# Kernel tuning notes

Hardware: AMD Instinct MI355X
Metric: run time of the kernel (lower is better)

Reference implementation:

```python
import jax, jax.numpy as jnp
import numpy as np
import math

B, S, D = 2, 2048, 1024
H, HKV = 16, 4
HD = D // H
NREP = H // HKV
E, TOPK, SHARED = 8, 2, 1
HIDDEN = 684
AUX_COEF = 0.01
RMS_EPS = 1e-5


def setup_inputs() -> dict:
    key = jax.random.key(0)
    ks = jax.random.split(key, 14)
    def w(k, shape):
        return jax.random.normal(k, shape, jnp.float32) * 0.02
    # standard RoPE angles, base 10000
    t = jnp.arange(S, dtype=jnp.float32)
    inv = 1.0 / (10000.0 ** (jnp.arange(0, HD, 2, dtype=jnp.float32) / HD))
    ang = t[:, None] * inv[None, :]  # [S, HD//2]
    return {
        "x": jax.random.normal(ks[0], (B, S, D), jnp.float32),
        "freqs_cos": jnp.cos(ang),
        "freqs_sin": jnp.sin(ang),
        "wq": w(ks[1], (D, D)),
        "wk": w(ks[2], (D, HKV * HD)),
        "wv": w(ks[3], (D, HKV * HD)),
        "wo": w(ks[4], (D, D)),
        "router_w": w(ks[5], (D, E)),
        "ew1": w(ks[6], (E, D, HIDDEN)),
        "ew2": w(ks[7], (E, HIDDEN, D)),
        "ew3": w(ks[8], (E, D, HIDDEN)),
        "sw1": w(ks[9], (SHARED, D, HIDDEN)),
        "sw2": w(ks[10], (SHARED, HIDDEN, D)),
        "sw3": w(ks[11], (SHARED, D, HIDDEN)),
        "g_attn": jnp.ones((D,), jnp.float32),
        "g_ffn": jnp.ones((D,), jnp.float32),
        "start_pos": 0,
    }


def rmsnorm(x, g, eps=RMS_EPS):
    xf = x.astype(jnp.float32)
    n = xf * jax.lax.rsqrt(jnp.mean(xf * xf, axis=-1, keepdims=True) + eps)
    return g * n.astype(x.dtype)


def rope(x, cos, sin):
    # pairs are consecutive elements (view_as_complex of reshape(..., -1, 2))
    xr, xi = x[..., 0::2], x[..., 1::2]
    c = cos[None, :, None, :]  # [1,S,1,HD//2]
    s = sin[None, :, None, :]
    r = xr * c - xi * s
    i = xr * s + xi * c
    return jnp.stack([r, i], axis=-1).reshape(x.shape)


def attention(x, freqs_cos, freqs_sin, wq, wk, wv, wo):
    b, s, d = x.shape
    q = (x @ wq).reshape(b, s, H, HD)
    k = (x @ wk).reshape(b, s, HKV, HD)
    v = (x @ wv).reshape(b, s, HKV, HD)
    q = rope(q, freqs_cos, freqs_sin)
    k = rope(k, freqs_cos, freqs_sin)
    k = jnp.repeat(k, NREP, axis=2)
    v = jnp.repeat(v, NREP, axis=2)
    q, k, v = (t.transpose(0, 2, 1, 3) for t in (q, k, v))  # [B,H,S,HD]
    att = jnp.einsum('bhqd,bhkd->bhqk', q, k) * (1.0 / math.sqrt(HD))
    # faithful to torch: tril then masked_fill(att == 0, -inf)
    tri = jnp.tril(jnp.ones((s, s), bool))
    att = jnp.where(tri, att, 0.0)
    att = jnp.where(att == 0.0, -jnp.inf, att)
    att = jax.nn.softmax(att, axis=-1)
    out = jnp.einsum('bhqk,bhkd->bhqd', att, v)
    out = out.transpose(0, 2, 1, 3).reshape(b, s, d)
    return out @ wo


def moe(x, router_w, ew1, ew2, ew3, sw1, sw2, sw3):
    b, s, d = x.shape
    xf = x.reshape(-1, d)                       # [N, D]
    logits = xf @ router_w                      # [N, E]
    probs = jax.nn.softmax(logits, axis=-1)
    _, topk_idx = jax.lax.top_k(logits, TOPK)   # [N, K]
    topk_p, _ = jax.lax.top_k(probs, TOPK)      # same ordering (softmax monotone)
    density = jnp.mean(jax.nn.one_hot(topk_idx[:, 0], E, dtype=jnp.float32), axis=0)
    aux = AUX_COEF * jnp.sum(density * jnp.mean(probs, axis=0)) * E
    # per-token combine weight over experts [N, E]
    onehot = jax.nn.one_hot(topk_idx, E, dtype=xf.dtype)  # [N, K, E]
    cw = jnp.einsum('nk,nke->ne', topk_p, onehot)
    # dense expert evaluation (jit-friendly dispatch/combine equivalent)
    h = jax.nn.silu(jnp.einsum('nd,edh->neh', xf, ew1)) * jnp.einsum('nd,edh->neh', xf, ew3)
    eo = jnp.einsum('neh,ehd->ned', h, ew2)
    out = jnp.einsum('ne,ned->nd', cw, eo)
    for i in range(SHARED):
        out = out + (jax.nn.silu(xf @ sw1[i]) * (xf @ sw3[i])) @ sw2[i]
    return out.reshape(b, s, d), aux


def reference(x, freqs_cos, freqs_sin, wq, wk, wv, wo, router_w, ew1, ew2, ew3, sw1, sw2, sw3, g_attn, g_ffn, start_pos):
    h = x + attention(rmsnorm(x, g_attn), freqs_cos, freqs_sin, wq, wk, wv, wo)
    ffn_out, aux = moe(rmsnorm(h, g_ffn), router_w, ew1, ew2, ew3, sw1, sw2, sw3)
    return h + ffn_out, aux
```

## Files before the change

### kernel.cpp

```cpp
#include <hip/hip_runtime.h>
#include <hip/hip_bf16.h>
#include <cstdint>

#define B_ 2
#define S_ 2048
#define D_ 1024
#define H_ 16
#define HKV_ 4
#define HD_ 64
#define E_ 8
#define HIDDEN_ 684
#define NT_ (B_*S_)
#define NEGBIG (-1e30f)

using bf16 = __hip_bfloat16;
typedef __attribute__((ext_vector_type(8))) short short8v;
typedef __attribute__((ext_vector_type(4))) short short4v;
typedef __attribute__((ext_vector_type(4))) float f32x4;

static __device__ __forceinline__ float b2f(bf16 v){ return __bfloat162float(v); }
static __device__ __forceinline__ bf16 f2b(float v){ return __float2bfloat16(v); }
static __device__ __forceinline__ short f2bs(float v){ bf16 h = f2b(v); return *reinterpret_cast<short*>(&h); }
static __device__ __forceinline__ float dload(const void* p, size_t i, int isbf){
  return isbf ? b2f(((const bf16*)p)[i]) : ((const float*)p)[i];
}

__global__ void k_detect(const uint32_t* __restrict__ g, int* __restrict__ flag, int* __restrict__ cnt){
  if(threadIdx.x == 0 && blockIdx.x == 0){
    uint32_t w0 = g[0], w1 = g[1], w2 = g[2], w3 = g[3];
    int bf;
    if(w0==0x3F803F80u && w1==0x3F803F80u && w2==0x3F803F80u && w3==0x3F803F80u) bf = 1;
    else if(w0==0x3F800000u && w1==0x3F800000u && w2==0x3F800000u && w3==0x3F800000u) bf = 0;
    else bf = 1;
    flag[0] = bf;
  }
  if(threadIdx.x < E_ && blockIdx.x == 0) cnt[threadIdx.x] = 0;
}

__global__ __launch_bounds__(256) void k_rms(const void* __restrict__ X, const void* __restrict__ g,
                                             bf16* __restrict__ outb, float* __restrict__ outf,
                                             const int* __restrict__ flag, int xdyn){
  int isbf = flag[0]; int xb = xdyn ? isbf : 0;
  int t = blockIdx.x; int tid = threadIdx.x;
  float v[4]; float ss = 0.f;
  #pragma unroll
  for(int i=0;i<4;i++){ v[i] = dload(X, (size_t)t*D_ + tid + i*256, xb); ss += v[i]*v[i]; }
  __shared__ float red[256];
  red[tid] = ss; __syncthreads();
  for(int st=128; st>0; st>>=1){ if(tid<st) red[tid] += red[tid+st]; __syncthreads(); }
  float r = rsqrtf(red[0]*(1.f/(float)D_) + 1e-5f);
  #pragma unroll
  for(int i=0;i<4;i++){
    int d = tid + i*256;
    float val = v[i]*r*dload(g, d, isbf);
    outb[(size_t)t*D_ + d] = f2b(val);
    if(outf) outf[(size_t)t*D_ + d] = val;
  }
}

#define ASTRIDE 40

static __device__ __forceinline__ f32x4 mfma16(short8v a, short8v b, f32x4 c){
  return __builtin_amdgcn_mfma_f32_16x16x32_bf16(a, b, c, 0, 0, 0);
}

template<int AMAP, int OMODE>
__global__ __launch_bounds__(256) void k_mgemm(
    const bf16* __restrict__ A, const void* __restrict__ Bw, void* __restrict__ Cout,
    const void* __restrict__ resid,
    int M, int N, int K, int ldc,
    const int* __restrict__ cnt, const int* __restrict__ offs, const int* __restrict__ list,
    const int* __restrict__ flag)
{
  int isbf = flag[0];
  int e, ct, rt;
  int base = 0; size_t eoff = 0;
  if(cnt){
    e = blockIdx.x;
    int nc = (N+63)>>6;
    ct = blockIdx.y % nc; rt = blockIdx.y / nc;
    M = cnt[e]; if(M<0) M=0; if(M>NT_) M=NT_;
    base = offs[e];
    eoff = (size_t)e*(size_t)K*(size_t)N;
  } else {
    e = 0; ct = blockIdx.x; rt = blockIdx.y;
  }
  int m0 = rt*128; if(m0 >= M) return;
  int n0 = ct*64;

  __shared__ short As[2][128*ASTRIDE];
  __shared__ short Bs[2][64*ASTRIDE];
  __shared__ int rowA[128];

  int tid = threadIdx.x;
  int w = tid>>6, l = tid&63, lr = l&15, lg = l>>4;

  if(tid < 128){
    int rloc = m0 + tid;
    int ar = -1;
    if(rloc < M) ar = (AMAP==2) ? (list[e*NT_ + rloc]>>1) : (base + rloc);
    rowA[tid] = ar;
  }
  __syncthreads();

  int srow = tid>>1, skh = (tid&1)*16;
  int keya = (srow>>4)&3, kb0 = skh>>3;
  int bk = tid>>3, bnc = (tid&7)*8;
  int keyb = ((tid&7)>>1)&3;
  int bcol = (((bk>>3)^keyb)<<3) + (bk&7);
  int arow = rowA[srow];

  short8v rA0, rA1, rB;

  auto loadAB = [&](int kt){
    int k0 = kt*32;
    {
      short tmp[16];
      if(arow >= 0 && k0+skh+16 <= K){
        const short4v* src = (const short4v*)(A + (size_t)arow*K + k0 + skh);
        #pragma unroll
        for(int c=0;c<4;c++) *(short4v*)&tmp[c*4] = src[c];
      } else {
        #pragma unroll
        for(int i=0;i<16;i++){
          int gk = k0+skh+i;
          short v = 0;
          if(arow>=0 && gk<K) v = *(const short*)&A[(size_t)arow*K+gk];
          tmp[i] = v;
        }
      }
      #pragma unroll
      for(int i=0;i<8;i++){ rA0[i]=tmp[i]; rA1[i]=tmp[8+i]; }
    }
    {
      int gk = k0 + bk;
      short tmp[8];
      if(gk < K && n0+bnc+8 <= N){
        size_t bb = eoff + (size_t)gk*N + n0 + bnc;
        if(isbf){
          const short4v* src = (const short4v*)((const bf16*)Bw + bb);
          *(short4v*)&tmp[0] = src[0];
          *(short4v*)&tmp[4] = src[1];
        } else {
          const f32x4* src = (const f32x4*)((const float*)Bw + bb);
          f32x4 f0 = src[0], f1 = src[1];
          #pragma unroll
          for(int i=0;i<4;i++){ tmp[i]=f2bs(f0[i]); tmp[4+i]=f2bs(f1[i]); }
        }
      } else {
        #pragma unroll
        for(int i=0;i<8;i++){
          int gn = n0+bnc+i;
          float v = 0.f;
          if(gk<K && gn<N) v = dload(Bw, eoff + (size_t)gk*N + gn, isbf);
          tmp[i] = f2bs(v);
        }
      }
      #pragma unroll
      for(int i=0;i<8;i++) rB[i]=tmp[i];
    }
  };
  auto writeAB = [&](int buf){
    *(short8v*)&As[buf][srow*ASTRIDE + ((kb0^keya)<<3)]     = rA0;
    *(short8v*)&As[buf][srow*ASTRIDE + (((kb0+1)^keya)<<3)] = rA1;
    #pragma unroll
    for(int i=0;i<8;i++) Bs[buf][(bnc+i)*ASTRIDE + bcol] = rB[i];
  };

  f32x4 acc[2][4] = {};
  int KT = (K+31)>>5;

  loadAB(0); writeAB(0);
  __syncthreads();
  int cur = 0;
  for(int kt=0; kt<KT; ++kt){
    bool more = (kt+1 < KT);
    if(more) loadAB(kt+1);
    short8v a[2], b[4];
    #pragma unroll
    for(int fi=0;fi<2;fi++)
      a[fi] = *(const short8v*)&As[cur][(w*32+fi*16+lr)*ASTRIDE + ((lg^((w*2+fi)&3))<<3)];
    #pragma unroll
    for(int fj=0;fj<4;fj++)
      b[fj] = *(const short8v*)&Bs[cur][(fj*16+lr)*ASTRIDE + ((lg^fj)<<3)];
    #pragma unroll
    for(int fi=0;fi<2;fi++)
      #pragma unroll
      for(int fj=0;fj<4;fj++)
        acc[fi][fj] = mfma16(a[fi], b[fj], acc[fi][fj]);
    if(more){ writeAB(cur^1); cur ^= 1; }
    __syncthreads();
  }

  #pragma unroll
  for(int fi=0;fi<2;fi++){
    #pragma unroll
    for(int r=0;r<4;r++){
      int rl = m0 + w*32 + fi*16 + lg*4 + r;
      if(rl >= M) continue;
      int orow;
      if(OMODE==2){ orow = list[e*NT_ + rl]; if(orow<0||orow>=2*NT_) continue; }
      else orow = base + rl;
      #pragma unroll
      for(int fj=0;fj<4;fj++){
        int gcol = n0 + fj*16 + lr;
        if(gcol >= N) continue;
        float v = acc[fi][fj][r];
        size_t o = (size_t)orow*ldc + gcol;
        if(OMODE==1)      ((float*)Cout)[o] = v + dload(resid, o, isbf);
        else if(OMODE==2) ((bf16*)Cout)[o] = f2b(v);
        else if(OMODE==3) ((float*)Cout)[o] = ((float*)Cout)[o] + v;
        else              ((bf16*)Cout)[o] = f2b(v);
      }
    }
  }
}

__global__ __launch_bounds__(256) void k_qkv(
    const bf16* __restrict__ A, const void* __restrict__ Wq, const void* __restrict__ Wk,
    const void* __restrict__ Wv, bf16* __restrict__ Oq, bf16* __restrict__ Ok, bf16* __restrict__ Ov,
    const void* __restrict__ fc, const void* __restrict__ fs,
    const int* __restrict__ flag)
{
  int isbf = flag[0];
  int ct = blockIdx.x, rt = blockIdx.y;
  const void* Bw; bf16* Cout; int N, n0;
  if(ct < 16){ Bw = Wq; Cout = Oq; N = D_;  n0 = ct*64; }
  else if(ct < 20){ Bw = Wk; Cout = Ok; N = 256; n0 = (ct-16)*64; }
  else { Bw = Wv; Cout = Ov; N = 256; n0 = (ct-20)*64; }
  const int K = D_, M = NT_;
  int m0 = rt*128;
  int dorope = (ct < 20);

  __shared__ short As[2][128*ASTRIDE];
  __shared__ short Bs[2][64*ASTRIDE];

  int tid = threadIdx.x;
  int w = tid>>6, l = tid&63, lr = l&15, lg = l>>4;

  int srow = tid>>1, skh = (tid&1)*16;
  int keya = (srow>>4)&3, kb0 = skh>>3;
  int bk = tid>>3, bnc = (tid&7)*8;
  int keyb = ((tid&7)>>1)&3;
  int bcol = (((bk>>3)^keyb)<<3) + (bk&7);
  int arow = m0 + srow;

  short8v rA0, rA1, rB;

  auto loadAB = [&](int kt){
    int k0 = kt*32;
    {
      short tmp[16];
      const short4v* src = (const short4v*)(A + (size_t)arow*K + k0 + skh);
      #pragma unroll
      for(int c=0;c<4;c++) *(short4v*)&tmp[c*4] = src[c];
      #pragma unroll
      for(int i=0;i<8;i++){ rA0[i]=tmp[i]; rA1[i]=tmp[8+i]; }
    }
    {
      int gk = k0 + bk;
      short tmp[8];
      size_t bb = (size_t)gk*N + n0 + bnc;
      if(isbf){
        const short4v* src = (const short4v*)((const bf16*)Bw + bb);
        *(short4v*)&tmp[0] = src[0];
        *(short4v*)&tmp[4] = src[1];
      } else {
        const f32x4* src = (const f32x4*)((const float*)Bw + bb);
        f32x4 f0 = src[0], f1 = src[1];
        #pragma unroll
        for(int i=0;i<4;i++){ tmp[i]=f2bs(f0[i]); tmp[4+i]=f2bs(f1[i]); }
      }
      #pragma unroll
      for(int i=0;i<8;i++) rB[i]=tmp[i];
    }
  };
  auto writeAB = [&](int buf){
    *(short8v*)&As[buf][srow*ASTRIDE + ((kb0^keya)<<3)]     = rA0;
    *(short8v*)&As[buf][srow*ASTRIDE + (((kb0+1)^keya)<<3)] = rA1;
    #pragma unroll
    for(int i=0;i<8;i++) Bs[buf][(bnc+i)*ASTRIDE + bcol] = rB[i];
  };

  f32x4 acc[2][4] = {};
  int KT = K>>5;

  loadAB(0); writeAB(0);
  __syncthreads();
  int cur = 0;
  for(int kt=0; kt<KT; ++kt){
    bool more = (kt+1 < KT);
    if(more) loadAB(kt+1);
    short8v a[2], b[4];
    #pragma unroll
    for(int fi=0;fi<2;fi++)
      a[fi] = *(const short8v*)&As[cur][(w*32+fi*16+lr)*ASTRIDE + ((lg^((w*2+fi)&3))<<3)];
    #pragma unroll
    for(int fj=0;fj<4;fj++)
      b[fj] = *(const short8v*)&Bs[cur][(fj*16+lr)*ASTRIDE + ((lg^fj)<<3)];
    #pragma unroll
    for(int fi=0;fi<2;fi++)
      #pragma unroll
      for(int fj=0;fj<4;fj++)
        acc[fi][fj] = mfma16(a[fi], b[fj], acc[fi][fj]);
    if(more){ writeAB(cur^1); cur ^= 1; }
    __syncthreads();
  }

  #pragma unroll
  for(int fi=0;fi<2;fi++){
    #pragma unroll
    for(int r=0;r<4;r++){
      int rl = m0 + w*32 + fi*16 + lg*4 + r;
      int s = rl & (S_-1);
      #pragma unroll
      for(int fj=0;fj<4;fj++){
        int gcol = n0 + fj*16 + lr;
        float v = acc[fi][fj][r];
        if(dorope){
          float partner = __shfl_xor(v, 1, 64);
          int p = (gcol & 63) >> 1;
          float c = dload(fc, s*32 + p, isbf);
          float sn = dload(fs, s*32 + p, isbf);
          if((l & 1) == 0) v = v*c - partner*sn;
          else             v = partner*sn + v*c;
        }
        Cout[(size_t)rl*N + gcol] = f2b(v);
      }
    }
  }
}

__global__ __launch_bounds__(256) void k_ffn1m(
    const bf16* __restrict__ A, const void* __restrict__ W1e, const void* __restrict__ W3e,
    const void* __restrict__ W1s, const void* __restrict__ W3s,
    bf16* __restrict__ OutE, bf16* __restrict__ OutS,
    const int* __restrict__ cnt, const int* __restrict__ offs, const int* __restrict__ list,
    const int* __restrict__ flag)
{
  int isbf = flag[0];
  const int K = D_, N = HIDDEN_;
  int e = blockIdx.x, y = blockIdx.y;
  int ct, rt, M, base, gat;
  const void* W1; const void* W3; bf16* Out;
  size_t eoff;
  if(y < 352){
    ct = y % 11; rt = y / 11;
    M = cnt[e]; if(M<0) M=0; if(M>NT_) M=NT_;
    base = offs[e]; gat = 1;
    W1 = W1e; W3 = W3e; Out = OutE;
    eoff = (size_t)e*(size_t)K*(size_t)N;
  } else {
    int ys = (y-352)*8 + e;
    ct = ys % 11; rt = ys / 11;
    M = NT_; base = 0; gat = 0;
    W1 = W1s; W3 = W3s; Out = OutS;
    eoff = 0;
  }
  int m0 = rt*128; if(m0 >= M) return;
  int n0 = ct*64;

  __shared__ short As[2][128*ASTRIDE];
  __shared__ short B1s[2][64*ASTRIDE];
  __shared__ short B3s[2][64*ASTRIDE];
  __shared__ int rowA[128];

  int tid = threadIdx.x;
  int w = tid>>6, l = tid&63, lr = l&15, lg = l>>4;

  if(tid < 128){
    int rloc = m0 + tid;
    int ar = -1;
    if(rloc < M) ar = gat ? (list[e*NT_ + rloc]>>1) : rloc;
    rowA[tid] = ar;
  }
  __syncthreads();

  int srow = tid>>1, skh = (tid&1)*16;
  int keya = (srow>>4)&3, kb0 = skh>>3;
  int bk = tid>>3, bnc = (tid&7)*8;
  int keyb = ((tid&7)>>1)&3;
  int bcol = (((bk>>3)^keyb)<<3) + (bk&7);
  int arow = rowA[srow];

  short8v rA0, rA1, rB1, rB3;

  auto loadB = [&](const void* Bw, int kt, short8v& rB){
    int k0 = kt*32;
    int gk = k0 + bk;
    short tmp[8];
    if(gk < K && n0+bnc+8 <= N){
      size_t bb = eoff + (size_t)gk*N + n0 + bnc;
      if(isbf){
        const short4v* src = (const short4v*)((const bf16*)Bw + bb);
        *(short4v*)&tmp[0] = src[0];
        *(short4v*)&tmp[4] = src[1];
      } else {
        const f32x4* src = (const f32x4*)((const float*)Bw + bb);
        f32x4 f0 = src[0], f1 = src[1];
        #pragma unroll
        for(int i=0;i<4;i++){ tmp[i]=f2bs(f0[i]); tmp[4+i]=f2bs(f1[i]); }
      }
    } else {
      #pragma unroll
      for(int i=0;i<8;i++){
        int gn = n0+bnc+i;
        float v = 0.f;
        if(gk<K && gn<N) v = dload(Bw, eoff + (size_t)gk*N + gn, isbf);
        tmp[i] = f2bs(v);
      }
    }
    #pragma unroll
    for(int i=0;i<8;i++) rB[i]=tmp[i];
  };
  auto loadA = [&](int kt){
    int k0 = kt*32;
    short tmp[16];
    if(arow >= 0 && k0+skh+16 <= K){
      const short4v* src = (const short4v*)(A + (size_t)arow*K + k0 + skh);
      #pragma unroll
      for(int c=0;c<4;c++) *(short4v*)&tmp[c*4] = src[c];
    } else {
      #pragma unroll
      for(int i=0;i<16;i++){
        int gk = k0+skh+i;
        short v = 0;
        if(arow>=0 && gk<K) v = *(const short*)&A[(size_t)arow*K+gk];
        tmp[i] = v;
      }
    }
    #pragma unroll
    for(int i=0;i<8;i++){ rA0[i]=tmp[i]; rA1[i]=tmp[8+i]; }
  };
  auto writeAll = [&](int buf){
    *(short8v*)&As[buf][srow*ASTRIDE + ((kb0^keya)<<3)]     = rA0;
    *(short8v*)&As[buf][srow*ASTRIDE + (((kb0+1)^keya)<<3)] = rA1;
    #pragma unroll
    for(int i=0;i<8;i++){
      B1s[buf][(bnc+i)*ASTRIDE + bcol] = rB1[i];
      B3s[buf][(bnc+i)*ASTRIDE + bcol] = rB3[i];
    }
  };

  f32x4 a1[2][4] = {}, a3[2][4] = {};
  int KT = (K+31)>>5;

  loadA(0); loadB(W1, 0, rB1); loadB(W3, 0, rB3); writeAll(0);
  __syncthreads();
  int cur = 0;
  for(int kt=0; kt<KT; ++kt){
    bool more = (kt+1 < KT);
    if(more){ loadA(kt+1); loadB(W1, kt+1, rB1); loadB(W3, kt+1, rB3); }
    short8v a[2], b1[4], b3[4];
    #pragma unroll
    for(int fi=0;fi<2;fi++)
      a[fi] = *(const short8v*)&As[cur][(w*32+fi*16+lr)*ASTRIDE + ((lg^((w*2+fi)&3))<<3)];
    #pragma unroll
    for(int fj=0;fj<4;fj++){
      b1[fj] = *(const short8v*)&B1s[cur][(fj*16+lr)*ASTRIDE + ((lg^fj)<<3)];
      b3[fj] = *(const short8v*)&B3s[cur][(fj*16+lr)*ASTRIDE + ((lg^fj)<<3)];
    }
    #pragma unroll
    for(int fi=0;fi<2;fi++)
      #pragma unroll
      for(int fj=0;fj<4;fj++){
        a1[fi][fj] = mfma16(a[fi], b1[fj], a1[fi][fj]);
        a3[fi][fj] = mfma16(a[fi], b3[fj], a3[fi][fj]);
      }
    if(more){ writeAll(cur^1); cur ^= 1; }
    __syncthreads();
  }

  #pragma unroll
  for(int fi=0;fi<2;fi++){
    #pragma unroll
    for(int r=0;r<4;r++){
      int rl = m0 + w*32 + fi*16 + lg*4 + r;
      if(rl >= M) continue;
      int orow = base + rl;
      #pragma unroll
      for(int fj=0;fj<4;fj++){
        int gcol = n0 + fj*16 + lr;
        if(gcol >= N) continue;
        float sg = a1[fi][fj][r];
        float v = (sg/(1.f+__expf(-sg))) * a3[fi][fj][r];
        Out[(size_t)orow*N + gcol] = f2b(v);
      }
    }
  }
}

__global__ __launch_bounds__(256) void k_ffn2m(
    const bf16* __restrict__ Ae, const bf16* __restrict__ Ash,
    const void* __restrict__ W2e, const void* __restrict__ W2s,
    bf16* __restrict__ OutE, float* __restrict__ OutS,
    const int* __restrict__ cnt, const int* __restrict__ offs, const int* __restrict__ list,
    const int* __restrict__ flag)
{
  int isbf = flag[0];
  const int K = HIDDEN_, N = D_;
  int e = blockIdx.x, y = blockIdx.y;
  int ct, rt, M, base, exm;
  const bf16* A; const void* Bw;
  size_t eoff;
  if(y < 256){
    ct = y % 8; rt = y / 8;
    M = cnt[e]; if(M<0) M=0; if(M>NT_) M=NT_;
    base = offs[e]; exm = 1;
    A = Ae; Bw = W2e;
    eoff = (size_t)e*(size_t)K*(size_t)N;
  } else {
    int ys = (y-256)*8 + e;
    ct = ys % 8; rt = ys / 8;
    M = NT_; base = 0; exm = 0;
    A = Ash; Bw = W2s;
    eoff = 0;
  }
  int m0 = rt*128; if(m0 >= M) return;
  int n0 = ct*128;

  __shared__ short As[128*ASTRIDE];
  __shared__ short Bs[128*ASTRIDE];

  int tid = threadIdx.x;
  int w = tid>>6, l = tid&63, lr = l&15, lg = l>>4;

  int srow = tid>>1, skh = (tid&1)*16;
  int keya = (srow>>4)&3, kb0 = skh>>3;
  int bk = tid>>3, bnc = (tid&7)*16;
  int keyb = (tid&7)&3;
  int bcol = (((bk>>3)^keyb)<<3) + (bk&7);
  int arow = (m0 + srow < M) ? (base + m0 + srow) : -1;

  short8v rA0, rA1, rB0v, rB1v;

  auto loadAB = [&](int kt){
    int k0 = kt*32;
    {
      short tmp[16];
      if(arow >= 0 && k0+skh+16 <= K){
        const short4v* src = (const short4v*)(A + (size_t)arow*K + k0 + skh);
        #pragma unroll
        for(int c=0;c<4;c++) *(short4v*)&tmp[c*4] = src[c];
      } else {
        #pragma unroll
        for(int i=0;i<16;i++){
          int gk = k0+skh+i;
          short v = 0;
          if(arow>=0 && gk<K) v = *(const short*)&A[(size_t)arow*K+gk];
          tmp[i] = v;
        }
      }
      #pragma unroll
      for(int i=0;i<8;i++){ rA0[i]=tmp[i]; rA1[i]=tmp[8+i]; }
    }
    {
      int gk = k0 + bk;
      short tmp[16];
      if(gk < K){
        size_t bb = eoff + (size_t)gk*N + n0 + bnc;
        if(isbf){
          const short4v* src = (const short4v*)((const bf16*)Bw + bb);
          #pragma unroll
          for(int c=0;c<4;c++) *(short4v*)&tmp[c*4] = src[c];
        } else {
          const f32x4* src = (const f32x4*)((const float*)Bw + bb);
          #pragma unroll
          for(int c=0;c<4;c++){
            f32x4 f = src[c];
            #pragma unroll
            for(int i=0;i<4;i++) tmp[c*4+i] = f2bs(f[i]);
          }
        }
      } else {
        #pragma unroll
        for(int i=0;i<16;i++) tmp[i] = 0;
      }
      #pragma unroll
      for(int i=0;i<8;i++){ rB0v[i]=tmp[i]; rB1v[i]=tmp[8+i]; }
    }
  };
  auto writeAB = [&](){
    *(short8v*)&As[srow*ASTRIDE + ((kb0^keya)<<3)]     = rA0;
    *(short8v*)&As[srow*ASTRIDE + (((kb0+1)^keya)<<3)] = rA1;
    #pragma unroll
    for(int i=0;i<8;i++) Bs[(bnc+i)*ASTRIDE + bcol]   = rB0v[i];
    #pragma unroll
    for(int i=0;i<8;i++) Bs[(bnc+8+i)*ASTRIDE + bcol] = rB1v[i];
  };

  f32x4 acc[2][8] = {};
  int KT = (K+31)>>5;

  loadAB(0); writeAB();
  __syncthreads();
  for(int kt=0; kt<KT; ++kt){
    bool more = (kt+1 < KT);
    if(more) loadAB(kt+1);
    short8v a[2], b[8];
    #pragma unroll
    for(int fi=0;fi<2;fi++)
      a[fi] = *(const short8v*)&As[(w*32+fi*16+lr)*ASTRIDE + ((lg^((w*2+fi)&3))<<3)];
    #pragma unroll
    for(int fj=0;fj<8;fj++)
      b[fj] = *(const short8v*)&Bs[(fj*16+lr)*ASTRIDE + ((lg^(fj&3))<<3)];
    #pragma unroll
    for(int fi=0;fi<2;fi++)
      #pragma unroll
      for(int fj=0;fj<8;fj++)
        acc[fi][fj] = mfma16(a[fi], b[fj], acc[fi][fj]);
    __syncthreads();
    if(more){ writeAB(); __syncthreads(); }
  }

  #pragma unroll
  for(int fi=0;fi<2;fi++){
    #pragma unroll
    for(int r=0;r<4;r++){
      int rl = m0 + w*32 + fi*16 + lg*4 + r;
      if(rl >= M) continue;
      if(exm){
        int orow = list[e*NT_ + rl];
        if(orow<0||orow>=2*NT_) continue;
        #pragma unroll
        for(int fj=0;fj<8;fj++){
          int gcol = n0 + fj*16 + lr;
          OutE[(size_t)orow*N + gcol] = f2b(acc[fi][fj][r]);
        }
      } else {
        #pragma unroll
        for(int fj=0;fj<8;fj++){
          int gcol = n0 + fj*16 + lr;
          size_t o = (size_t)rl*N + gcol;
          OutS[o] = OutS[o] + acc[fi][fj][r];
        }
      }
    }
  }
}

#define TST 72

__global__ __launch_bounds__(256) void k_attn(const bf16* __restrict__ Q, const bf16* __restrict__ Kg,
                                              const bf16* __restrict__ V, bf16* __restrict__ Out){
  int qt_ = (S_/64 - 1) - blockIdx.x;
  int h = blockIdx.y, b = blockIdx.z;
  int kvh = h>>2;
  const bf16* qb = Q + (size_t)b*S_*D_ + h*HD_;
  const bf16* kb = Kg + (size_t)b*S_*256 + kvh*HD_;
  const bf16* vb = V  + (size_t)b*S_*256 + kvh*HD_;
  __shared__ short Qs[64*TST];
  __shared__ short Ks[64*TST];
  __shared__ short Vt[64*TST];
  __shared__ short Ps[4][16*TST];
  int tid = threadIdx.x;
  int w = tid>>6, l = tid&63, lr = l&15, lg = l>>4;
  int sr = tid>>2, sc0 = (tid&3)*16;
  int vc = (((sr>>3)^(tid&3))<<3) + (sr&7);

  {
    const short8v* src = (const short8v*)(qb + (size_t)(qt_*64 + sr)*D_ + sc0);
    *(short8v*)&Qs[sr*TST + sc0]     = src[0];
    *(short8v*)&Qs[sr*TST + sc0 + 8] = src[1];
  }
  __syncthreads();
  short8v aQ0 = *(const short8v*)&Qs[(w*16+lr)*TST + lg*8];
  short8v aQ1 = *(const short8v*)&Qs[(w*16+lr)*TST + lg*8 + 32];

  float mreg[4], lreg[4];
  f32x4 accO[4] = {};
  #pragma unroll
  for(int r=0;r<4;r++){ mreg[r] = NEGBIG; lreg[r] = 0.f; }

  for(int kt=0; kt<=qt_; ++kt){
    __syncthreads();
    {
      const short8v* ksrc = (const short8v*)(kb + (size_t)(kt*64 + sr)*256 + sc0);
      *(short8v*)&Ks[sr*TST + sc0]     = ksrc[0];
      *(short8v*)&Ks[sr*TST + sc0 + 8] = ksrc[1];
      const short8v* vsrc = (const short8v*)(vb + (size_t)(kt*64 + sr)*256 + sc0);
      short8v v0 = vsrc[0], v1 = vsrc[1];
      #pragma unroll
      for(int i=0;i<8;i++){
        Vt[(sc0+i)*TST + vc]   = v0[i];
        Vt[(sc0+8+i)*TST + vc] = v1[i];
      }
    }
    __syncthreads();
    f32x4 s[4];
    #pragma unroll
    for(int fj=0; fj<4; fj++){
      short8v b0 = *(const short8v*)&Ks[(fj*16+lr)*TST + lg*8];
      short8v b1 = *(const short8v*)&Ks[(fj*16+lr)*TST + lg*8 + 32];
      f32x4 z = {};
      z = mfma16(aQ0, b0, z);
      z = mfma16(aQ1, b1, z);
      s[fj] = z;
    }
    #pragma unroll
    for(int fj=0; fj<4; fj++)
      #pragma unroll
      for(int r=0;r<4;r++){
        float v = s[fj][r]*0.125f;
        if(kt==qt_ && (fj*16+lr) > (w*16+lg*4+r)) v = NEGBIG;
        s[fj][r] = v;
      }
    float p[4][4], sc[4];
    #pragma unroll
    for(int r=0;r<4;r++){
      float mx = fmaxf(fmaxf(s[0][r],s[1][r]), fmaxf(s[2][r],s[3][r]));
      mx = fmaxf(mx, __shfl_xor(mx,1,64));
      mx = fmaxf(mx, __shfl_xor(mx,2,64));
      mx = fmaxf(mx, __shfl_xor(mx,4,64));
      mx = fmaxf(mx, __shfl_xor(mx,8,64));
      float mn = fmaxf(mreg[r], mx);
      sc[r] = __expf(mreg[r]-mn);
      float ps = 0.f;
      #pragma unroll
      for(int fj=0;fj<4;fj++){ float pv = __expf(s[fj][r]-mn); p[fj][r] = pv; ps += pv; }
      ps += __shfl_xor(ps,1,64); ps += __shfl_xor(ps,2,64);
      ps += __shfl_xor(ps,4,64); ps += __shfl_xor(ps,8,64);
      lreg[r] = lreg[r]*sc[r] + ps;
      mreg[r] = mn;
    }
    #pragma unroll
    for(int fj=0;fj<4;fj++)
      #pragma unroll
      for(int r=0;r<4;r++)
        accO[fj][r] *= sc[r];
    #pragma unroll
    for(int fj=0;fj<4;fj++)
      #pragma unroll
      for(int r=0;r<4;r++)
        Ps[w][(lg*4+r)*TST + fj*16+lr] = f2bs(p[fj][r]);
    short8v a0 = *(const short8v*)&Ps[w][lr*TST + lg*8];
    short8v a1 = *(const short8v*)&Ps[w][lr*TST + lg*8 + 32];
    #pragma unroll
    for(int fj=0;fj<4;fj++){
      int row = fj*16+lr;
      short8v b0 = *(const short8v*)&Vt[row*TST + ((lg^fj)<<3)];
      short8v b1 = *(const short8v*)&Vt[row*TST + (((lg^fj)+4)<<3)];
      accO[fj] = mfma16(a0, b0, accO[fj]);
      accO[fj] = mfma16(a1, b1, accO[fj]);
    }
  }
  #pragma unroll
  for(int r=0;r<4;r++){
    int qr = qt_*64 + w*16 + lg*4 + r;
    float inv = (lreg[r] > 0.f) ? 1.f/lreg[r] : 0.f;
    #pragma unroll
    for(int fj=0;fj<4;fj++)
      Out[((size_t)(b*S_+qr))*D_ + h*HD_ + fj*16+lr] = f2b(accO[fj][r]*inv);
  }
}

__global__ __launch_bounds__(64) void k_router(const float* __restrict__ X, const void* __restrict__ W,
                                               float* __restrict__ probs, float* __restrict__ p01,
                                               int* __restrict__ idx0buf, int* __restrict__ list,
                                               int* __restrict__ cnt, const int* __restrict__ flag){
  int isbf = flag[0];
  int t = blockIdx.x; int lane = threadIdx.x;
  float pe[8] = {};
  if(isbf){
    const bf16* Wb = (const bf16*)W;
    for(int d = lane; d < D_; d += 64){
      float xv = X[(size_t)t*D_ + d];
      #pragma unroll
      for(int e=0;e<8;e++) pe[e] += xv*b2f(Wb[(size_t)d*E_+e]);
    }
  } else {
    const float* Wf = (const float*)W;
    for(int d = lane; d < D_; d += 64){
      float xv = X[(size_t)t*D_ + d];
      #pragma unroll
      for(int e=0;e<8;e++) pe[e] += xv*Wf[(size_t)d*E_+e];
    }
  }
  for(int msk=1;msk<64;msk<<=1)
    #pragma unroll
    for(int e=0;e<8;e++) pe[e] += __shfl_xor(pe[e], msk, 64);
  if(lane == 0){
    float mx = pe[0];
    #pragma unroll
    for(int e=1;e<8;e++) mx = fmaxf(mx, pe[e]);
    float pr[8], sum = 0.f;
    #pragma unroll
    for(int e=0;e<8;e++){ pr[e] = __expf(pe[e]-mx); sum += pr[e]; }
    #pragma unroll
    for(int e=0;e<8;e++){ pr[e] /= sum; probs[t*8+e] = pr[e]; }
    int i0 = 0;
    #pragma unroll
    for(int e=1;e<8;e++) if(pe[e] > pe[i0]) i0 = e;
    int i1 = -1;
    #pragma unroll
    for(int e=0;e<8;e++){ if(e==i0) continue; if(i1<0 || pe[e] > pe[i1]) i1 = e; }
    p01[t*2]   = pr[i0];
    p01[t*2+1] = pr[i1];
    idx0buf[t] = i0;
    int pos = atomicAdd(&cnt[i0], 1);
    if(pos >= 0 && pos < NT_) list[i0*NT_ + pos] = t*2;
    pos     = atomicAdd(&cnt[i1], 1);
    if(pos >= 0 && pos < NT_) list[i1*NT_ + pos] = t*2 + 1;
  }
}

__global__ __launch_bounds__(256) void k_stats(const float* __restrict__ probs, const int* __restrict__ idx0buf,
                                               float* __restrict__ cnt0f, float* __restrict__ psum){
  int e = blockIdx.x; int tid = threadIdx.x;
  float sp = 0.f, sc = 0.f;
  for(int n = tid; n < NT_; n += 256){ sp += probs[n*8+e]; sc += (idx0buf[n]==e) ? 1.f : 0.f; }
  __shared__ float r1[256], r2[256];
  r1[tid] = sp; r2[tid] = sc; __syncthreads();
  for(int st=128; st>0; st>>=1){ if(tid<st){ r1[tid]+=r1[tid+st]; r2[tid]+=r2[tid+st]; } __syncthreads(); }
  if(tid==0){ psum[e] = r1[0]; cnt0f[e] = r2[0]; }
}

__global__ void k_finish(const float* __restrict__ cnt0f, const float* __restrict__ psum,
                         const int* __restrict__ cnt, int* __restrict__ offs,
                         bf16* __restrict__ auxb, float* __restrict__ auxf, const int* __restrict__ flag){
  if(threadIdx.x==0 && blockIdx.x==0){
    int o = 0;
    for(int e=0;e<8;e++){ offs[e] = o; int c = cnt[e]; if(c < 0) c = 0; if(c > NT_) c = NT_; o += c; }
    float aux = 0.f;
    for(int e=0;e<8;e++) aux += (cnt0f[e]*(1.f/(float)NT_))*(psum[e]*(1.f/(float)NT_));
    float v = aux*0.01f*8.f;
    if(flag[0]) auxb[0] = f2b(v); else auxf[0] = v;
  }
}

__global__ __launch_bounds__(256) void k_combine(const float* __restrict__ hbuf, const bf16* __restrict__ eosl,
                                                 const float* __restrict__ p01,
                                                 bf16* __restrict__ outb, float* __restrict__ outf,
                                                 const int* __restrict__ flag){
  int t = blockIdx.x; int tid = threadIdx.x;
  int isbf = flag[0];
  float p0 = p01[t*2], p1 = p01[t*2+1];
  #pragma unroll
  for(int i=0;i<4;i++){
    int d = tid + i*256;
    float v = hbuf[(size_t)t*D_ + d]
            + p0*b2f(eosl[((size_t)(t*2))*D_ + d])
            + p1*b2f(eosl[((size_t)(t*2+1))*D_ + d]);
    size_t o = (size_t)t*D_ + d;
    if(isbf) outb[o] = f2b(v); else outf[o] = v;
  }
}

static const size_t O_HBUF = 0;
static const size_t O_XNB  = 16777216;
static const size_t O_QLIN = 25165824;
static const size_t O_KLIN = 33554432;
static const size_t O_VLIN = 35651584;
static const size_t O_AOUT = 37748736;
static const size_t O_XN2B = 16777216;
static const size_t O_XN2F = 25165824;
static const size_t O_HEXP = 46137344;
static const size_t O_SHH  = 57344000;
static const size_t O_EOSL = 16777216;
static const size_t O_PROBS= 62947328;
static const size_t O_P01  = 63078400;
static const size_t O_IDX0 = 63111168;
static const size_t O_LIST = 63127552;
static const size_t O_CNT  = 63258624;
static const size_t O_CNT0 = 63258656;
static const size_t O_PSUM = 63258688;
static const size_t O_OFFS = 63258720;
static const size_t O_FLAG = 63258752;

extern "C" void kernel_launch(void* const* d_in, const int* in_sizes, int n_in,
                              void* d_out, int out_size, void* d_ws, size_t ws_size,
                              hipStream_t stream){
  (void)in_sizes; (void)n_in; (void)out_size; (void)ws_size;
  char* ws = (char*)d_ws;
  float* hbuf = (float*)(ws + O_HBUF);
  bf16* xnb   = (bf16*)(ws + O_XNB);
  bf16* qlin  = (bf16*)(ws + O_QLIN);
  bf16* klin  = (bf16*)(ws + O_KLIN);
  bf16* vlin  = (bf16*)(ws + O_VLIN);
  bf16* aout  = (bf16*)(ws + O_AOUT);
  bf16* xn2b  = (bf16*)(ws + O_XN2B);
  float* xn2f = (float*)(ws + O_XN2F);
  bf16* hexp  = (bf16*)(ws + O_HEXP);
  bf16* shh   = (bf16*)(ws + O_SHH);
  bf16* eosl  = (bf16*)(ws + O_EOSL);
  float* probs=(float*)(ws + O_PROBS);
  float* p01 = (float*)(ws + O_P01);
  int*  idx0 = (int*)(ws + O_IDX0);
  int*  list = (int*)(ws + O_LIST);
  int*  cnt  = (int*)(ws + O_CNT);
  float* cnt0f=(float*)(ws + O_CNT0);
  float* psum= (float*)(ws + O_PSUM);
  int*  offs = (int*)(ws + O_OFFS);
  int*  flg  = (int*)(ws + O_FLAG);

  bf16* outb = (bf16*)d_out;
  float* outf = (float*)d_out;
  bf16* auxb = outb + (size_t)NT_*D_;
  float* auxf = outf + (size_t)NT_*D_;

  k_detect<<<1, 64, 0, stream>>>((const uint32_t*)d_in[14], flg, cnt);

  k_rms<<<NT_, 256, 0, stream>>>(d_in[0], d_in[14], xnb, nullptr, flg, 1);

  k_qkv<<<dim3(24,32), 256, 0, stream>>>(xnb, d_in[3], d_in[4], d_in[5], qlin, klin, vlin,
                                         d_in[1], d_in[2], flg);

  k_attn<<<dim3(S_/64, H_, B_), 256, 0, stream>>>(qlin, klin, vlin, aout);

  k_mgemm<0,1><<<dim3(16,32), 256, 0, stream>>>(aout, d_in[6], hbuf, d_in[0], NT_, D_, D_, D_, nullptr, nullptr, nullptr, flg);

  k_rms<<<NT_, 256, 0, stream>>>(hbuf, d_in[15], xn2b, xn2f, flg, 0);

  k_router<<<NT_, 64, 0, stream>>>(xn2f, d_in[7], probs, p01, idx0, list, cnt, flg);
  k_stats<<<E_, 256, 0, stream>>>(probs, idx0, cnt0f, psum);
  k_finish<<<1, 64, 0, stream>>>(cnt0f, psum, cnt, offs, auxb, auxf, flg);

  k_ffn1m<<<dim3(E_, 352+44), 256, 0, stream>>>(xn2b, d_in[8], d_in[10], d_in[11], d_in[13],
                                                hexp, shh, cnt, offs, list, flg);

  k_ffn2m<<<dim3(E_, 256+32), 256, 0, stream>>>(hexp, shh, d_in[9], d_in[12],
                                                eosl, hbuf, cnt, offs, list, flg);

  k_combine<<<NT_, 256, 0, stream>>>(hbuf, eosl, p01, outb, outf, flg);
}
```

Measured before the change: 617.2 us.

## Widen QKV and Wo GEMM tiles to 128x128 with single-buffered LDS

The QKV projection and the output-projection GEMMs now use 128x128 output tiles instead of 128x64, so each wave holds twice as many accumulators and each A tile is reused across more columns. Shared memory drops from double to single buffering, with an extra barrier before writing the next tile. The generic templated k_mgemm is replaced by a specialized k_wo kernel with no bounds checks. The trade-off is fewer blocks (384 and 256) on a large GPU, higher register pressure, and less overlap between loads and MFMA.

```diff
diff --git a/kernel.cpp b/kernel.cpp
--- a/kernel.cpp
+++ b/kernel.cpp
@@ -64,132 +64,93 @@
   return __builtin_amdgcn_mfma_f32_16x16x32_bf16(a, b, c, 0, 0, 0);
 }
 
-template<int AMAP, int OMODE>
-__global__ __launch_bounds__(256) void k_mgemm(
-    const bf16* __restrict__ A, const void* __restrict__ Bw, void* __restrict__ Cout,
-    const void* __restrict__ resid,
-    int M, int N, int K, int ldc,
-    const int* __restrict__ cnt, const int* __restrict__ offs, const int* __restrict__ list,
-    const int* __restrict__ flag)
+__global__ __launch_bounds__(256) void k_wo(
+    const bf16* __restrict__ A, const void* __restrict__ Bw, float* __restrict__ Cout,
+    const void* __restrict__ resid, const int* __restrict__ flag)
 {
   int isbf = flag[0];
-  int e, ct, rt;
-  int base = 0; size_t eoff = 0;
-  if(cnt){
-    e = blockIdx.x;
-    int nc = (N+63)>>6;
-    ct = blockIdx.y % nc; rt = blockIdx.y / nc;
-    M = cnt[e]; if(M<0) M=0; if(M>NT_) M=NT_;
-    base = offs[e];
-    eoff = (size_t)e*(size_t)K*(size_t)N;
-  } else {
-    e = 0; ct = blockIdx.x; rt = blockIdx.y;
-  }
-  int m0 = rt*128; if(m0 >= M) return;
-  int n0 = ct*64;
-
-  __shared__ short As[2][128*ASTRIDE];
-  __shared__ short Bs[2][64*ASTRIDE];
-  __shared__ int rowA[128];
+  const int K = D_, N = D_, M = NT_;
+  int ct = blockIdx.x, rt = blockIdx.y;
+  int m0 = rt*128;
+  int n0 = ct*128;
+
+  __shared__ short As[128*ASTRIDE];
+  __shared__ short Bs[128*ASTRIDE];
 
   int tid = threadIdx.x;
   int w = tid>>6, l = tid&63, lr = l&15, lg = l>>4;
 
-  if(tid < 128){
-    int rloc = m0 + tid;
-    int ar = -1;
-    if(rloc < M) ar = (AMAP==2) ? (list[e*NT_ + rloc]>>1) : (base + rloc);
-    rowA[tid] = ar;
-  }
-  __syncthreads();
-
   int srow = tid>>1, skh = (tid&1)*16;
   int keya = (srow>>4)&3, kb0 = skh>>3;
-  int bk = tid>>3, bnc = (tid&7)*8;
-  int keyb = ((tid&7)>>1)&3;
+  int bk = tid>>3, bnc = (tid&7)*16;
+  int keyb = (tid&7)&3;
   int bcol = (((bk>>3)^keyb)<<3) + (bk&7);
-  int arow = rowA[srow];
-
-  short8v rA0, rA1, rB;
+  int arow = m0 + srow;
+
+  short8v rA0, rA1, rB0v, rB1v;
 
   auto loadAB = [&](int kt){
     int k0 = kt*32;
     {
       short tmp[16];
-      if(arow >= 0 && k0+skh+16 <= K){
-        const short4v* src = (const short4v*)(A + (size_t)arow*K + k0 + skh);
+      const short4v* src = (const short4v*)(A + (size_t)arow*K + k0 + skh);
+      #pragma unroll
+      for(int c=0;c<4;c++) *(short4v*)&tmp[c*4] = src[c];
+      #pragma unroll
+      for(int i=0;i<8;i++){ rA0[i]=tmp[i]; rA1[i]=tmp[8+i]; }
+    }
+    {
+      int gk = k0 + bk;
+      short tmp[16];
+      size_t bb = (size_t)gk*N + n0 + bnc;
+      if(isbf){
+        const short4v* src = (const short4v*)((const bf16*)Bw + bb);
         #pragma unroll
         for(int c=0;c<4;c++) *(short4v*)&tmp[c*4] = src[c];
       } else {
-        #pragma unroll
-        for(int i=0;i<16;i++){
-          int gk = k0+skh+i;
-          short v = 0;
-          if(arow>=0 && gk<K) v = *(const short*)&A[(size_t)arow*K+gk];
-          tmp[i] = v;
+        const f32x4* src = (const f32x4*)((const float*)Bw + bb);
+        #pragma unroll
+        for(int c=0;c<4;c++){
+          f32x4 f = src[c];
+          #pragma unroll
+          for(int i=0;i<4;i++) tmp[c*4+i] = f2bs(f[i]);
         }
       }
       #pragma unroll
-      for(int i=0;i<8;i++){ rA0[i]=tmp[i]; rA1[i]=tmp[8+i]; }
-    }
-    {
-      int gk = k0 + bk;
-      short tmp[8];
-      if(gk < K && n0+bnc+8 <= N){
-        size_t bb = eoff + (size_t)gk*N + n0 + bnc;
-        if(isbf){
-          const short4v* src = (const short4v*)((const bf16*)Bw + bb);
-          *(short4v*)&tmp[0] = src[0];
-          *(short4v*)&tmp[4] = src[1];
-        } else {
-          const f32x4* src = (const f32x4*)((const float*)Bw + bb);
-          f32x4 f0 = src[0], f1 = src[1];
-          #pragma unroll
-          for(int i=0;i<4;i++){ tmp[i]=f2bs(f0[i]); tmp[4+i]=f2bs(f1[i]); }
-        }
-      } else {
-        #pragma unroll
-        for(int i=0;i<8;i++){
-          int gn = n0+bnc+i;
-          float v = 0.f;
-          if(gk<K && gn<N) v = dload(Bw, eoff + (size_t)gk*N + gn, isbf);
-          tmp[i] = f2bs(v);
-        }
-      }
-      #pragma unroll
-      for(int i=0;i<8;i++) rB[i]=tmp[i];
+      for(int i=0;i<8;i++){ rB0v[i]=tmp[i]; rB1v[i]=tmp[8+i]; }
     }
   };
-  auto writeAB = [&](int buf){
-    *(short8v*)&As[buf][srow*ASTRIDE + ((kb0^keya)<<3)]     = rA0;
-    *(short8v*)&As[buf][srow*ASTRIDE + (((kb0+1)^keya)<<3)] = rA1;
-    #pragma unroll
-    for(int i=0;i<8;i++) Bs[buf][(bnc+i)*ASTRIDE + bcol] = rB[i];
+  auto writeAB = [&](){
+    *(short8v*)&As[srow*ASTRIDE + ((kb0^keya)<<3)]     = rA0;
+    *(short8v*)&As[srow*ASTRIDE + (((kb0+1)^keya)<<3)] = rA1;
+    #pragma unroll
+    for(int i=0;i<8;i++) Bs[(bnc+i)*ASTRIDE + bcol]   = rB0v[i];
+    #pragma unroll
+    for(int i=0;i<8;i++) Bs[(bnc+8+i)*ASTRIDE + bcol] = rB1v[i];
   };
 
-  f32x4 acc[2][4] = {};
-  int KT = (K+31)>>5;
-
-  loadAB(0); writeAB(0);
+  f32x4 acc[2][8] = {};
+  int KT = K>>5;
+
+  loadAB(0); writeAB();
   __syncthreads();
-  int cur = 0;
   for(int kt=0; kt<KT; ++kt){
     bool more = (kt+1 < KT);
     if(more) loadAB(kt+1);
-    short8v a[2], b[4];
+    short8v a[2], b[8];
     #pragma unroll
     for(int fi=0;fi<2;fi++)
-      a[fi] = *(const short8v*)&As[cur][(w*32+fi*16+lr)*ASTRIDE + ((lg^((w*2+fi)&3))<<3)];
-    #pragma unroll
-    for(int fj=0;fj<4;fj++)
-      b[fj] = *(const short8v*)&Bs[cur][(fj*16+lr)*ASTRIDE + ((lg^fj)<<3)];
+      a[fi] = *(const short8v*)&As[(w*32+fi*16+lr)*ASTRIDE + ((lg^((w*2+fi)&3))<<3)];
+    #pragma unroll
+    for(int fj=0;fj<8;fj++)
+      b[fj] = *(const short8v*)&Bs[(fj*16+lr)*ASTRIDE + ((lg^(fj&3))<<3)];
     #pragma unroll
     for(int fi=0;fi<2;fi++)
       #pragma unroll
-      for(int fj=0;fj<4;fj++)
+      for(int fj=0;fj<8;fj++)
         acc[fi][fj] = mfma16(a[fi], b[fj], acc[fi][fj]);
-    if(more){ writeAB(cur^1); cur ^= 1; }
     __syncthreads();
+    if(more){ writeAB(); __syncthreads(); }
   }
 
   #pragma unroll
@@ -197,20 +158,11 @@
     #pragma unroll
     for(int r=0;r<4;r++){
       int rl = m0 + w*32 + fi*16 + lg*4 + r;
-      if(rl >= M) continue;
-      int orow;
-      if(OMODE==2){ orow = list[e*NT_ + rl]; if(orow<0||orow>=2*NT_) continue; }
-      else orow = base + rl;
-      #pragma unroll
-      for(int fj=0;fj<4;fj++){
+      #pragma unroll
+      for(int fj=0;fj<8;fj++){
         int gcol = n0 + fj*16 + lr;
-        if(gcol >= N) continue;
-        float v = acc[fi][fj][r];
-        size_t o = (size_t)orow*ldc + gcol;
-        if(OMODE==1)      ((float*)Cout)[o] = v + dload(resid, o, isbf);
-        else if(OMODE==2) ((bf16*)Cout)[o] = f2b(v);
-        else if(OMODE==3) ((float*)Cout)[o] = ((float*)Cout)[o] + v;
-        else              ((bf16*)Cout)[o] = f2b(v);
+        size_t o = (size_t)rl*N + gcol;
+        Cout[o] = acc[fi][fj][r] + dload(resid, o, isbf);
       }
     }
   }
@@ -225,27 +177,27 @@
   int isbf = flag[0];
   int ct = blockIdx.x, rt = blockIdx.y;
   const void* Bw; bf16* Cout; int N, n0;
-  if(ct < 16){ Bw = Wq; Cout = Oq; N = D_;  n0 = ct*64; }
-  else if(ct < 20){ Bw = Wk; Cout = Ok; N = 256; n0 = (ct-16)*64; }
-  else { Bw = Wv; Cout = Ov; N = 256; n0 = (ct-20)*64; }
+  if(ct < 8){ Bw = Wq; Cout = Oq; N = D_;  n0 = ct*128; }
+  else if(ct < 10){ Bw = Wk; Cout = Ok; N = 256; n0 = (ct-8)*128; }
+  else { Bw = Wv; Cout = Ov; N = 256; n0 = (ct-10)*128; }
   const int K = D_, M = NT_;
   int m0 = rt*128;
-  int dorope = (ct < 20);
-
-  __shared__ short As[2][128*ASTRIDE];
-  __shared__ short Bs[2][64*ASTRIDE];
+  int dorope = (ct < 10);
+
+  __shared__ short As[128*ASTRIDE];
+  __shared__ short Bs[128*ASTRIDE];
 
   int tid = threadIdx.x;
   int w = tid>>6, l = tid&63, lr = l&15, lg = l>>4;
 
   int srow = tid>>1, skh = (tid&1)*16;
   int keya = (srow>>4)&3, kb0 = skh>>3;
-  int bk = tid>>3, bnc = (tid&7)*8;
-  int keyb = ((tid&7)>>1)&3;
+  int bk = tid>>3, bnc = (tid&7)*16;
+  int keyb = (tid&7)&3;
   int bcol = (((bk>>3)^keyb)<<3) + (bk&7);
   int arow = m0 + srow;
 
-  short8v rA0, rA1, rB;
+  short8v rA0, rA1, rB0v, rB1v;
 
   auto loadAB = [&](int kt){
     int k0 = kt*32;
@@ -259,52 +211,56 @@
     }
     {
       int gk = k0 + bk;
-      short tmp[8];
+      short tmp[16];
       size_t bb = (size_t)gk*N + n0 + bnc;
       if(isbf){
         const short4v* src = (const short4v*)((const bf16*)Bw + bb);
-        *(short4v*)&tmp[0] = src[0];
-        *(short4v*)&tmp[4] = src[1];
+        #pragma unroll
+        for(int c=0;c<4;c++) *(short4v*)&tmp[c*4] = src[c];
       } else {
         const f32x4* src = (const f32x4*)((const float*)Bw + bb);
-        f32x4 f0 = src[0], f1 = src[1];
-        #pragma unroll
-        for(int i=0;i<4;i++){ tmp[i]=f2bs(f0[i]); tmp[4+i]=f2bs(f1[i]); }
-      }
-      #pragma unroll
-      for(int i=0;i<8;i++) rB[i]=tmp[i];
+        #pragma unroll
+        for(int c=0;c<4;c++){
+          f32x4 f = src[c];
+          #pragma unroll
+          for(int i=0;i<4;i++) tmp[c*4+i] = f2bs(f[i]);
+        }
+      }
+      #pragma unroll
+      for(int i=0;i<8;i++){ rB0v[i]=tmp[i]; rB1v[i]=tmp[8+i]; }
     }
   };
-  auto writeAB = [&](int buf){
-    *(short8v*)&As[buf][srow*ASTRIDE + ((kb0^keya)<<3)]     = rA0;
-    *(short8v*)&As[buf][srow*ASTRIDE + (((kb0+1)^keya)<<3)] = rA1;
-    #pragma unroll
-    for(int i=0;i<8;i++) Bs[buf][(bnc+i)*ASTRIDE + bcol] = rB[i];
+  auto writeAB = [&](){
+    *(short8v*)&As[srow*ASTRIDE + ((kb0^keya)<<3)]     = rA0;
+    *(short8v*)&As[srow*ASTRIDE + (((kb0+1)^keya)<<3)] = rA1;
+    #pragma unroll
+    for(int i=0;i<8;i++) Bs[(bnc+i)*ASTRIDE + bcol]   = rB0v[i];
+    #pragma unroll
+    for(int i=0;i<8;i++) Bs[(bnc+8+i)*ASTRIDE + bcol] = rB1v[i];
   };
 
-  f32x4 acc[2][4] = {};
+  f32x4 acc[2][8] = {};
   int KT = K>>5;
 
-  loadAB(0); writeAB(0);
+  loadAB(0); writeAB();
   __syncthreads();
-  int cur = 0;
   for(int kt=0; kt<KT; ++kt){
     bool more = (kt+1 < KT);
     if(more) loadAB(kt+1);
-    short8v a[2], b[4];
+    short8v a[2], b[8];
     #pragma unroll
     for(int fi=0;fi<2;fi++)
-      a[fi] = *(const short8v*)&As[cur][(w*32+fi*16+lr)*ASTRIDE + ((lg^((w*2+fi)&3))<<3)];
-    #pragma unroll
-    for(int fj=0;fj<4;fj++)
-      b[fj] = *(const short8v*)&Bs[cur][(fj*16+lr)*ASTRIDE + ((lg^fj)<<3)];
+      a[fi] = *(const short8v*)&As[(w*32+fi*16+lr)*ASTRIDE + ((lg^((w*2+fi)&3))<<3)];
+    #pragma unroll
+    for(int fj=0;fj<8;fj++)
+      b[fj] = *(const short8v*)&Bs[(fj*16+lr)*ASTRIDE + ((lg^(fj&3))<<3)];
     #pragma unroll
     for(int fi=0;fi<2;fi++)
       #pragma unroll
-      for(int fj=0;fj<4;fj++)
+      for(int fj=0;fj<8;fj++)
         acc[fi][fj] = mfma16(a[fi], b[fj], acc[fi][fj]);
-    if(more){ writeAB(cur^1); cur ^= 1; }
     __syncthreads();
+    if(more){ writeAB(); __syncthreads(); }
   }
 
   #pragma unroll
@@ -314,7 +270,7 @@
       int rl = m0 + w*32 + fi*16 + lg*4 + r;
       int s = rl & (S_-1);
       #pragma unroll
-      for(int fj=0;fj<4;fj++){
+      for(int fj=0;fj<8;fj++){
         int gcol = n0 + fj*16 + lr;
         float v = acc[fi][fj][r];
         if(dorope){
@@ -902,12 +858,12 @@
 
   k_rms<<<NT_, 256, 0, stream>>>(d_in[0], d_in[14], xnb, nullptr, flg, 1);
 
-  k_qkv<<<dim3(24,32), 256, 0, stream>>>(xnb, d_in[3], d_in[4], d_in[5], qlin, klin, vlin,
+  k_qkv<<<dim3(12,32), 256, 0, stream>>>(xnb, d_in[3], d_in[4], d_in[5], qlin, klin, vlin,
                                          d_in[1], d_in[2], flg);
 
   k_attn<<<dim3(S_/64, H_, B_), 256, 0, stream>>>(qlin, klin, vlin, aout);
 
-  k_mgemm<0,1><<<dim3(16,32), 256, 0, stream>>>(aout, d_in[6], hbuf, d_in[0], NT_, D_, D_, D_, nullptr, nullptr, nullptr, flg);
+  k_wo<<<dim3(8,32), 256, 0, stream>>>(aout, d_in[6], hbuf, d_in[0], flg);
 
   k_rms<<<NT_, 256, 0, stream>>>(hbuf, d_in[15], xn2b, xn2f, flg, 0);
 
```

Result: slower. 632.3 us (+2.4%).
